# Performance work log

Measured on AMD Instinct MI355X. Metric: run time of the kernel, lower is better.

Reference implementation:

```python
import jax, jax.numpy as jnp
import numpy as np

DIM = 768
B, S = 16, 1024
EPS = 1e-5


def setup_inputs() -> dict:
    key = jax.random.key(0)
    ks = jax.random.split(key, 13)
    std = 1.0 / np.sqrt(DIM)
    inp = {
        "x_A": jax.random.normal(ks[0], (B, S, DIM), jnp.float32),
        "x_B": jax.random.normal(ks[1], (B, S, DIM), jnp.float32),
        "x_C": jax.random.normal(ks[2], (B, S, DIM), jnp.float32),
        "W_q": jax.random.normal(ks[3], (DIM, DIM), jnp.float32) * std,
        "b_q": jax.random.normal(ks[4], (DIM,), jnp.float32) * std,
        "W_k": jax.random.normal(ks[5], (DIM, DIM), jnp.float32) * std,
        "b_k": jax.random.normal(ks[6], (DIM,), jnp.float32) * std,
        "W_v": jax.random.normal(ks[7], (DIM, DIM), jnp.float32) * std,
        "b_v": jax.random.normal(ks[8], (DIM,), jnp.float32) * std,
        "gamma": jnp.ones((DIM,), jnp.float32),
        "beta": jnp.zeros((DIM,), jnp.float32),
        "W_fc": jax.random.normal(ks[9], (DIM, DIM), jnp.float32) * std,
        "b_fc": jax.random.normal(ks[10], (DIM,), jnp.float32) * std,
    }
    return inp


def _linear(x, W, b):
    # torch nn.Linear: x @ W.T + b
    return jnp.einsum('bsd,ed->bse', x, W) + b


def _layernorm(x, gamma, beta):
    mu = jnp.mean(x, axis=-1, keepdims=True)
    var = jnp.mean((x - mu) ** 2, axis=-1, keepdims=True)
    return (x - mu) * jax.lax.rsqrt(var + EPS) * gamma + beta


def reference(x_A, x_B, x_C, W_q, b_q, W_k, b_k, W_v, b_v, gamma, beta, W_fc, b_fc):
    scale = 1.0 / jnp.sqrt(jnp.float32(DIM))
    Q = _linear(x_C, W_q, b_q)
    K_A = _linear(x_A, W_k, b_k)
    K_B = _linear(x_B, W_k, b_k)
    V_A = _linear(x_A, W_v, b_v)
    V_B = _linear(x_B, W_v, b_v)
    attn_A = jax.nn.softmax(jnp.einsum('bqd,bkd->bqk', Q, K_A) * scale, axis=-1)
    attn_B = jax.nn.softmax(jnp.einsum('bqd,bkd->bqk', Q, K_B) * scale, axis=-1)
    interp_A = jnp.einsum('bqk,bkd->bqd', attn_A, V_A)
    interp_B = jnp.einsum('bqk,bkd->bqd', attn_B, V_B)
    h = _layernorm(interp_A + interp_B + x_C, gamma, beta)
    return _linear(h, W_fc, b_fc)
```

## Files before the change

kernel.cpp:

```cpp
#include <hip/hip_runtime.h>

#define DIMV 768
#define BATCH 16
#define SEQ 1024
#define LN_EPS 1e-5f

typedef __attribute__((ext_vector_type(8))) short bf16x8;
typedef __attribute__((ext_vector_type(4))) float f32x4;
typedef unsigned short ushort_t;

__device__ __forceinline__ unsigned short f2bf(float f) {
    unsigned u = __float_as_uint(f);
    u = (u + 0x7FFFu + ((u >> 16) & 1u)) >> 16;
    return (unsigned short)u;
}

__global__ __launch_bounds__(256) void gemm_bf16_nt(
    const ushort_t* __restrict__ A, const ushort_t* __restrict__ B,
    const float* __restrict__ bias, const float* __restrict__ bias2,
    void* __restrict__ Cout, void* __restrict__ Cout2,
    int K, int lda, int ldb, int ldc, float scale, int mode,
    long long sAz, long long sBz, long long sCz, int CbArg)
{
    int bx = blockIdx.x, by = blockIdx.y, bz = blockIdx.z;
    {
        const unsigned Z  = gridDim.z;
        const unsigned nx = gridDim.x, ny = gridDim.y;
        if (Z > 1) {
            const unsigned nxy = nx * ny;
            const unsigned lid = ((unsigned)bz * ny + (unsigned)by) * nx + (unsigned)bx;
            unsigned r;
            if ((Z & 7u) == 0u) {
                const unsigned c  = lid & 7u;
                const unsigned rp = lid >> 3;
                bz = (int)(c + 8u * (rp / nxy));
                r  = rp % nxy;
            } else {
                bz = (int)(lid % Z);
                r  = lid / Z;
            }
            bx = (int)(r % nx);
            by = (int)(r / nx);
        } else {
            const unsigned nwg = nx * ny;
            if ((nwg & 7u) == 0u) {
                const unsigned lid = (unsigned)by * nx + (unsigned)bx;
                const unsigned nl  = (lid & 7u) * (nwg >> 3) + (lid >> 3);
                bx = (int)(nl % nx);
                by = (int)(nl / nx);
            }
        }
    }

    A += (long long)bz * sAz;
    B += (long long)bz * sBz;
    float*    Cf  = (float*)Cout    + ((mode == 0) ? (long long)bz * sCz : 0);
    ushort_t* Ch  = (ushort_t*)Cout + ((mode == 1) ? (long long)bz * sCz : 0);
    ushort_t* Ch2 = (ushort_t*)Cout2;

    __shared__ ushort_t As[4][128 * 32];
    __shared__ ushort_t Bs[4][128 * 32];

    const int t    = threadIdx.x;
    const int wave = t >> 6;
    const int lane = t & 63;
    const int quad = lane >> 4;
    const int lr   = lane & 15;
    const int wy   = wave >> 1;
    const int wx   = wave & 1;

    const int m0 = by * 128;
    const int n0 = bx * 128;

    const ushort_t* Abase = A + (long long)m0 * lda;
    const ushort_t* Bbase = B + (long long)n0 * ldb;

    auto issue = [&](int k0, int slot) {
        #pragma unroll
        for (int i = 0; i < 2; ++i) {
            const int idx = t + 256 * i;
            const int r   = idx >> 2;
            const int q   = idx & 3;
            const int c   = (q ^ ((r >> 1) & 3)) * 8;
            __builtin_amdgcn_global_load_lds(
                (const __attribute__((address_space(1))) unsigned int*)(Abase + (long long)r * lda + k0 + c),
                (__attribute__((address_space(3))) unsigned int*)&As[slot][idx * 8], 16, 0, 0);
            __builtin_amdgcn_global_load_lds(
                (const __attribute__((address_space(1))) unsigned int*)(Bbase + (long long)r * ldb + k0 + c),
                (__attribute__((address_space(3))) unsigned int*)&Bs[slot][idx * 8], 16, 0, 0);
        }
    };

    int offA[4], offB[4];
    #pragma unroll
    for (int i = 0; i < 4; ++i) {
        const int rowA = wy * 64 + i * 16 + lr;
        offA[i] = rowA * 32 + ((quad ^ ((rowA >> 1) & 3)) * 8);
        const int rowB = wx * 64 + i * 16 + lr;
        offB[i] = rowB * 32 + ((quad ^ ((rowB >> 1) & 3)) * 8);
    }

    f32x4 acc[4][4] = {};

    const int NK = K >> 5;
    issue(0, 0);
    issue(32, 1);
    for (int ki = 0; ki < NK; ++ki) {
        const int k2 = (ki + 2 < NK) ? (ki + 2) << 5 : (NK - 1) << 5;
        issue(k2, (ki + 2) & 3);
        asm volatile("s_waitcnt vmcnt(8)" ::: "memory");
        asm volatile("s_barrier" ::: "memory");

        const ushort_t* as = &As[ki & 3][0];
        const ushort_t* bs = &Bs[ki & 3][0];
        bf16x8 af[4], bfr[4];
        #pragma unroll
        for (int i = 0; i < 4; ++i) af[i]  = *(const bf16x8*)&as[offA[i]];
        #pragma unroll
        for (int j = 0; j < 4; ++j) bfr[j] = *(const bf16x8*)&bs[offB[j]];

        #pragma unroll
        for (int i = 0; i < 4; ++i)
            #pragma unroll
            for (int j = 0; j < 4; ++j)
                acc[i][j] = __builtin_amdgcn_mfma_f32_16x16x32_bf16(
                    af[i], bfr[j], acc[i][j], 0, 0, 0);
    }

    #pragma unroll
    for (int j = 0; j < 4; ++j) {
        const int n = n0 + wx * 64 + j * 16 + lr;
        float bv;
        if (mode == 4) bv = (n < DIMV) ? bias[n] : bias2[n - DIMV];
        else           bv = bias ? bias[n] : 0.0f;
        #pragma unroll
        for (int i = 0; i < 4; ++i) {
            #pragma unroll
            for (int r = 0; r < 4; ++r) {
                const int m = m0 + wy * 64 + i * 16 + quad * 4 + r;
                const float val = acc[i][j][r] * scale + bv;
                if (mode == 0) {
                    Cf[(long long)m * ldc + n] = val;
                } else if (mode == 1) {
                    Ch[(long long)m * ldc + n] = f2bf(val);
                } else {
                    const int bh = m >> 10, s = m & 1023;
                    const int hf = (bh >= CbArg) ? 1 : 0;
                    const int b  = bh - (hf ? CbArg : 0);
                    if (n < DIMV) {
                        Ch[(long long)b * (2 * SEQ * DIMV) + (long long)(hf * SEQ + s) * DIMV + n] = f2bf(val);
                    } else {
                        Ch2[(long long)b * (2 * SEQ * DIMV) + (long long)(n - DIMV) * (2 * SEQ) + hf * SEQ + s] = f2bf(val);
                    }
                }
            }
        }
    }
}

__global__ __launch_bounds__(256) void f32_to_bf16(
    const float* __restrict__ in, ushort_t* __restrict__ out)
{
    const long long i = ((long long)blockIdx.x * 256 + threadIdx.x) * 4;
    float4 v = *reinterpret_cast<const float4*>(in + i);
    ushort4 o;
    o.x = f2bf(v.x); o.y = f2bf(v.y); o.z = f2bf(v.z); o.w = f2bf(v.w);
    *reinterpret_cast<ushort4*>(out + i) = o;
}

__global__ __launch_bounds__(256) void softmax2_inplace(float* __restrict__ S)
{
    float* s = S + (long long)blockIdx.x * (2 * SEQ);
    const int t  = threadIdx.x;
    const int hf = t >> 7;
    const int tt = t & 127;
    const int base = hf * SEQ + tt * 8;
    __shared__ float red[256];

    float4 v0 = *reinterpret_cast<const float4*>(&s[base]);
    float4 v1 = *reinterpret_cast<const float4*>(&s[base + 4]);
    float mx = fmaxf(fmaxf(fmaxf(v0.x, v0.y), fmaxf(v0.z, v0.w)),
                     fmaxf(fmaxf(v1.x, v1.y), fmaxf(v1.z, v1.w)));
    red[t] = mx;
    __syncthreads();
    for (int st = 64; st > 0; st >>= 1) {
        if (tt < st) red[t] = fmaxf(red[t], red[t + st]);
        __syncthreads();
    }
    mx = red[hf << 7];
    __syncthreads();

    v0.x = __expf(v0.x - mx); v0.y = __expf(v0.y - mx);
    v0.z = __expf(v0.z - mx); v0.w = __expf(v0.w - mx);
    v1.x = __expf(v1.x - mx); v1.y = __expf(v1.y - mx);
    v1.z = __expf(v1.z - mx); v1.w = __expf(v1.w - mx);
    red[t] = (v0.x + v0.y + v0.z + v0.w) + (v1.x + v1.y + v1.z + v1.w);
    __syncthreads();
    for (int st = 64; st > 0; st >>= 1) {
        if (tt < st) red[t] += red[t + st];
        __syncthreads();
    }
    const float inv = 1.0f / red[hf << 7];

    ushort4 o0, o1;
    o0.x = f2bf(v0.x * inv); o0.y = f2bf(v0.y * inv);
    o0.z = f2bf(v0.z * inv); o0.w = f2bf(v0.w * inv);
    o1.x = f2bf(v1.x * inv); o1.y = f2bf(v1.y * inv);
    o1.z = f2bf(v1.z * inv); o1.w = f2bf(v1.w * inv);
    *reinterpret_cast<ushort4*>((ushort_t*)s + base)     = o0;
    *reinterpret_cast<ushort4*>((ushort_t*)s + base + 4) = o1;
}

__global__ __launch_bounds__(256) void add_layernorm(
    const float* __restrict__ ACC, const float* __restrict__ xC,
    const float* __restrict__ gamma, const float* __restrict__ beta,
    ushort_t* __restrict__ H)
{
    const long long row = blockIdx.x;
    const float* a = ACC + row * DIMV;
    const float* x = xC  + row * DIMV;
    ushort_t*    h = H   + row * DIMV;
    const int t = threadIdx.x;

    __shared__ float r1[256];
    __shared__ float r2[256];

    float vals[3];
    float s = 0.f, ss = 0.f;
    #pragma unroll
    for (int i = 0; i < 3; ++i) {
        const int j = t + i * 256;
        float v = a[j] + x[j];
        vals[i] = v;
        s += v; ss += v * v;
    }
    r1[t] = s; r2[t] = ss;
    __syncthreads();
    for (int st = 128; st > 0; st >>= 1) {
        if (t < st) { r1[t] += r1[t + st]; r2[t] += r2[t + st]; }
        __syncthreads();
    }
    const float mu  = r1[0] * (1.0f / DIMV);
    const float var = r2[0] * (1.0f / DIMV) - mu * mu;
    const float inv = rsqrtf(var + LN_EPS);

    #pragma unroll
    for (int i = 0; i < 3; ++i) {
        const int j = t + i * 256;
        h[j] = f2bf((vals[i] - mu) * inv * gamma[j] + beta[j]);
    }
}

extern "C" void kernel_launch(void* const* d_in, const int* in_sizes, int n_in,
                              void* d_out, int out_size, void* d_ws, size_t ws_size,
                              hipStream_t stream)
{
    const float* xA    = (const float*)d_in[0];
    const float* xB    = (const float*)d_in[1];
    const float* xC    = (const float*)d_in[2];
    const float* Wq    = (const float*)d_in[3];
    const float* bq    = (const float*)d_in[4];
    const float* Wk    = (const float*)d_in[5];
    const float* bk    = (const float*)d_in[6];
    const float* Wv    = (const float*)d_in[7];
    const float* bv    = (const float*)d_in[8];
    const float* gamma = (const float*)d_in[9];
    const float* beta  = (const float*)d_in[10];
    const float* Wfc   = (const float*)d_in[11];
    const float* bfc   = (const float*)d_in[12];
    float* out = (float*)d_out;

    const long long eW   = (long long)DIMV * DIMV;
    const long long perB = (long long)SEQ * DIMV;
    const long long perP = (long long)SEQ * SEQ;

    const long long wBytes        = 4 * eW * 2;
    const long long perBatchBytes = 14 * perB + 8 * perP;

    long long Cmax = ((long long)ws_size - wBytes) / perBatchBytes;
    if (Cmax > BATCH) Cmax = BATCH;
    if (Cmax < 1)     Cmax = 1;
    const int nChunks = (int)((BATCH + Cmax - 1) / Cmax);
    const int CbStd   = (BATCH + nChunks - 1) / nChunks;

    char* cur = (char*)d_ws;
    ushort_t* Wqb  = (ushort_t*)cur; cur += eW * 2;
    ushort_t* Wkvb = (ushort_t*)cur; cur += 2 * eW * 2;
    ushort_t* Wfcb = (ushort_t*)cur; cur += eW * 2;
    char* chunkBase = cur;

    const float scale = 0.03608439182435161f;

    f32_to_bf16<<<(int)(eW / 1024), 256, 0, stream>>>(Wq,  Wqb);
    f32_to_bf16<<<(int)(eW / 1024), 256, 0, stream>>>(Wk,  Wkvb);
    f32_to_bf16<<<(int)(eW / 1024), 256, 0, stream>>>(Wv,  Wkvb + eW);
    f32_to_bf16<<<(int)(eW / 1024), 256, 0, stream>>>(Wfc, Wfcb);

    for (int b0 = 0; b0 < BATCH; b0 += CbStd) {
        const int Cb = (b0 + CbStd <= BATCH) ? CbStd : (BATCH - b0);
        const long long off = (long long)b0 * perB;

        char* p = chunkBase;
        ushort_t* xABb = (ushort_t*)p;
        float*    ACC  = (float*)p;    p += (long long)Cb * 4 * perB;
        float*    Sf   = (float*)p;
        ushort_t* xCb  = (ushort_t*)p; p += (long long)Cb * 8 * perP;
        ushort_t* Qb   = (ushort_t*)p; p += (long long)Cb * 2 * perB;
        ushort_t* Kb   = (ushort_t*)p; p += (long long)Cb * 4 * perB;
        ushort_t* Vtb  = (ushort_t*)p; p += (long long)Cb * 4 * perB;

        dim3 gq  (DIMV / 128, Cb * (SEQ / 128), 1);
        dim3 gkv (2 * DIMV / 128, 2 * Cb * (SEQ / 128), 1);
        dim3 gsc2(2 * SEQ / 128, SEQ / 128, Cb);
        dim3 gpv (DIMV / 128, SEQ / 128, Cb);
        const int gcv = (int)((long long)Cb * perB / 1024);

        f32_to_bf16<<<gcv, 256, 0, stream>>>(xC + off, xCb);
        gemm_bf16_nt<<<gq, 256, 0, stream>>>(xCb, Wqb, bq, nullptr, Qb, nullptr,
            DIMV, DIMV, DIMV, DIMV, 1.f, 1, 0, 0, 0, 0);
        f32_to_bf16<<<gcv, 256, 0, stream>>>(xA + off, xABb);
        f32_to_bf16<<<gcv, 256, 0, stream>>>(xB + off, xABb + (long long)Cb * perB);
        gemm_bf16_nt<<<gkv, 256, 0, stream>>>(xABb, Wkvb, bk, bv, Kb, Vtb,
            DIMV, DIMV, DIMV, DIMV, 1.f, 4, 0, 0, 0, Cb);

        gemm_bf16_nt<<<gsc2, 256, 0, stream>>>(Qb, Kb, nullptr, nullptr, Sf, nullptr,
            DIMV, DIMV, DIMV, 2 * SEQ, scale, 0, perB, 2 * perB, 2 * perP, 0);

        softmax2_inplace<<<Cb * SEQ, 256, 0, stream>>>(Sf);

        gemm_bf16_nt<<<gpv, 256, 0, stream>>>((const ushort_t*)Sf, Vtb, nullptr, nullptr, ACC, nullptr,
            2 * SEQ, 4 * SEQ, 2 * SEQ, DIMV, 1.f, 0, 4 * perP, 2 * perB, perB, 0);

        add_layernorm<<<Cb * SEQ, 256, 0, stream>>>(ACC, xC + off, gamma, beta, Qb);

        gemm_bf16_nt<<<gq, 256, 0, stream>>>(Qb, Wfcb, bfc, nullptr, out + off, nullptr,
            DIMV, DIMV, DIMV, DIMV, 1.f, 0, 0, 0, 0, 0);
    }
}
```

Measured before the change: 732.8 us.

## Shrink GEMM LDS ring to three stages and sub-chunk attention workspace

The GEMM now uses a 3-slot LDS ring that prefetches one K-step ahead, in place of a 4-slot ring that prefetched two ahead. This lowers shared memory per block, which may raise occupancy, but exposes more global-load latency. The host workspace plan now aliases the fp32 accumulator with the K buffer. It also processes the score/softmax/PV stages in sub-chunks of at most 8 batches, so a larger batch chunk fits in the workspace and fewer outer chunks and launches are needed.

```diff
diff --git a/kernel.cpp b/kernel.cpp
--- a/kernel.cpp
+++ b/kernel.cpp
@@ -58,8 +58,8 @@
     ushort_t* Ch  = (ushort_t*)Cout + ((mode == 1) ? (long long)bz * sCz : 0);
     ushort_t* Ch2 = (ushort_t*)Cout2;
 
-    __shared__ ushort_t As[4][128 * 32];
-    __shared__ ushort_t Bs[4][128 * 32];
+    __shared__ ushort_t As[3][128 * 32];
+    __shared__ ushort_t Bs[3][128 * 32];
 
     const int t    = threadIdx.x;
     const int wave = t >> 6;
@@ -104,15 +104,15 @@
 
     const int NK = K >> 5;
     issue(0, 0);
-    issue(32, 1);
+    int cur = 0, nxt = 1;
     for (int ki = 0; ki < NK; ++ki) {
-        const int k2 = (ki + 2 < NK) ? (ki + 2) << 5 : (NK - 1) << 5;
-        issue(k2, (ki + 2) & 3);
-        asm volatile("s_waitcnt vmcnt(8)" ::: "memory");
+        const int kn = (ki + 1 < NK) ? (ki + 1) << 5 : 0;
+        issue(kn, nxt);
+        asm volatile("s_waitcnt vmcnt(4)" ::: "memory");
         asm volatile("s_barrier" ::: "memory");
 
-        const ushort_t* as = &As[ki & 3][0];
-        const ushort_t* bs = &Bs[ki & 3][0];
+        const ushort_t* as = &As[cur][0];
+        const ushort_t* bs = &Bs[cur][0];
         bf16x8 af[4], bfr[4];
         #pragma unroll
         for (int i = 0; i < 4; ++i) af[i]  = *(const bf16x8*)&as[offA[i]];
@@ -125,6 +125,9 @@
             for (int j = 0; j < 4; ++j)
                 acc[i][j] = __builtin_amdgcn_mfma_f32_16x16x32_bf16(
                     af[i], bfr[j], acc[i][j], 0, 0, 0);
+
+        cur = nxt;
+        nxt = (nxt == 2) ? 0 : nxt + 1;
     }
 
     #pragma unroll
@@ -274,13 +277,20 @@
     const long long perB = (long long)SEQ * DIMV;
     const long long perP = (long long)SEQ * SEQ;
 
-    const long long wBytes        = 4 * eW * 2;
-    const long long perBatchBytes = 14 * perB + 8 * perP;
-
-    long long Cmax = ((long long)ws_size - wBytes) / perBatchBytes;
-    if (Cmax > BATCH) Cmax = BATCH;
-    if (Cmax < 1)     Cmax = 1;
-    const int nChunks = (int)((BATCH + Cmax - 1) / Cmax);
+    const long long wBytes = 4 * eW * 2;
+
+    auto needBytes = [&](long long cb, long long sc) {
+        const long long s = 8 * perP * sc;
+        const long long x = 4 * perB * cb;
+        return (s > x ? s : x) + 10 * perB * cb;
+    };
+
+    int CbFit = 1;
+    for (int c = BATCH; c >= 1; --c) {
+        const long long sc = c < 8 ? c : 8;
+        if (wBytes + needBytes(c, sc) <= (long long)ws_size) { CbFit = c; break; }
+    }
+    const int nChunks = (BATCH + CbFit - 1) / CbFit;
     const int CbStd   = (BATCH + nChunks - 1) / nChunks;
 
     char* cur = (char*)d_ws;
@@ -300,19 +310,24 @@
         const int Cb = (b0 + CbStd <= BATCH) ? CbStd : (BATCH - b0);
         const long long off = (long long)b0 * perB;
 
+        int SC = Cb;
+        while (SC > 1 && wBytes + needBytes(Cb, SC) > (long long)ws_size) --SC;
+
+        const long long Sbytes =
+            (8 * perP * (long long)SC > 4 * perB * (long long)Cb)
+                ? 8 * perP * (long long)SC : 4 * perB * (long long)Cb;
+
         char* p = chunkBase;
+        ushort_t* xCb  = (ushort_t*)p;
         ushort_t* xABb = (ushort_t*)p;
-        float*    ACC  = (float*)p;    p += (long long)Cb * 4 * perB;
-        float*    Sf   = (float*)p;
-        ushort_t* xCb  = (ushort_t*)p; p += (long long)Cb * 8 * perP;
-        ushort_t* Qb   = (ushort_t*)p; p += (long long)Cb * 2 * perB;
-        ushort_t* Kb   = (ushort_t*)p; p += (long long)Cb * 4 * perB;
-        ushort_t* Vtb  = (ushort_t*)p; p += (long long)Cb * 4 * perB;
+        float*    Sf   = (float*)p;    p += Sbytes;
+        ushort_t* Qb   = (ushort_t*)p; p += 2 * perB * Cb;
+        ushort_t* Kb   = (ushort_t*)p;
+        float*    ACC  = (float*)p;    p += 4 * perB * Cb;
+        ushort_t* Vtb  = (ushort_t*)p; p += 4 * perB * Cb;
 
         dim3 gq  (DIMV / 128, Cb * (SEQ / 128), 1);
         dim3 gkv (2 * DIMV / 128, 2 * Cb * (SEQ / 128), 1);
-        dim3 gsc2(2 * SEQ / 128, SEQ / 128, Cb);
-        dim3 gpv (DIMV / 128, SEQ / 128, Cb);
         const int gcv = (int)((long long)Cb * perB / 1024);
 
         f32_to_bf16<<<gcv, 256, 0, stream>>>(xC + off, xCb);
@@ -323,13 +338,23 @@
         gemm_bf16_nt<<<gkv, 256, 0, stream>>>(xABb, Wkvb, bk, bv, Kb, Vtb,
             DIMV, DIMV, DIMV, DIMV, 1.f, 4, 0, 0, 0, Cb);
 
-        gemm_bf16_nt<<<gsc2, 256, 0, stream>>>(Qb, Kb, nullptr, nullptr, Sf, nullptr,
-            DIMV, DIMV, DIMV, 2 * SEQ, scale, 0, perB, 2 * perB, 2 * perP, 0);
-
-        softmax2_inplace<<<Cb * SEQ, 256, 0, stream>>>(Sf);
-
-        gemm_bf16_nt<<<gpv, 256, 0, stream>>>((const ushort_t*)Sf, Vtb, nullptr, nullptr, ACC, nullptr,
-            2 * SEQ, 4 * SEQ, 2 * SEQ, DIMV, 1.f, 0, 4 * perP, 2 * perB, perB, 0);
+        for (int s0 = 0; s0 < Cb; s0 += SC) {
+            const int sc = (s0 + SC <= Cb) ? SC : (Cb - s0);
+            dim3 gsc(2 * SEQ / 128, SEQ / 128, sc);
+            dim3 gpv(DIMV / 128, SEQ / 128, sc);
+
+            gemm_bf16_nt<<<gsc, 256, 0, stream>>>(
+                Qb + (long long)s0 * perB, Kb + (long long)s0 * 2 * perB,
+                nullptr, nullptr, Sf, nullptr,
+                DIMV, DIMV, DIMV, 2 * SEQ, scale, 0, perB, 2 * perB, 2 * perP, 0);
+
+            softmax2_inplace<<<sc * SEQ, 256, 0, stream>>>(Sf);
+
+            gemm_bf16_nt<<<gpv, 256, 0, stream>>>(
+                (const ushort_t*)Sf, Vtb + (long long)s0 * 2 * perB,
+                nullptr, nullptr, ACC + (long long)s0 * perB, nullptr,
+                2 * SEQ, 4 * SEQ, 2 * SEQ, DIMV, 1.f, 0, 4 * perP, 2 * perB, perB, 0);
+        }
 
         add_layernorm<<<Cb * SEQ, 256, 0, stream>>>(ACC, xC + off, gamma, beta, Qb);
 
```

Result: faster. 643.3 us (-12.2%).
